# Kernel tuning notes

Hardware: AMD Instinct MI355X
Metric: run time of the kernel (lower is better)

Reference implementation:

```python
import jax, jax.numpy as jnp
import numpy as np

B, N, K = 4, 16384, 8
NF = [8, 32, 64, 128, 256]
E = N * K


def setup_inputs() -> dict:
    key = jax.random.key(0)
    ks = jax.random.split(key, 16)
    x = jax.random.normal(ks[0], (B, N, NF[0]), jnp.float32)
    # knn-style edge list: every node appears as a center K times (no empty segments)
    centers = jnp.tile(jnp.repeat(jnp.arange(N), K)[None, None, :], (B, 1, 1))
    neighbors = jax.random.randint(ks[1], (B, 1, E), 0, N)
    edge_index = jnp.concatenate([centers, neighbors], axis=1)
    specs = [("0a", NF[0], NF[1]), ("0b", NF[0], NF[1]),
             ("1a", NF[1], NF[2]), ("1b", NF[1], NF[2]),
             ("2a", NF[2], NF[3]), ("2b", NF[2], NF[3]),
             ("3a", NF[3], NF[4]), ("3b", NF[3], NF[4]),
             ("cat", NF[1] + NF[2] + NF[3] + NF[4], 1)]
    inp = {"x": x, "edge_index": edge_index}
    for i, (nm, ci, co) in enumerate(specs):
        inp["W" + nm] = jax.random.normal(ks[2 + i], (ci, co), jnp.float32) / np.sqrt(ci)
        inp["g" + nm] = jnp.ones((co,), jnp.float32)   # BN gamma
        inp["b" + nm] = jnp.zeros((co,), jnp.float32)  # BN beta
    inp["bias"] = jnp.zeros((1,), jnp.float32)
    return inp


def _bn(x, g, b):
    # training-mode BatchNorm1d over all rows (GraphBatchNorm1d reduces over batch*num_points)
    m = x.mean(0)
    v = jnp.mean(jnp.square(x - m), 0)  # biased variance, as torch BN uses for normalization
    return g * (x - m) * jax.lax.rsqrt(v + 1e-5) + b


def _mlp(x, W, g, b):
    # Linear(bias=False) -> BN -> LeakyReLU(0.2)
    return jax.nn.leaky_relu(_bn(x @ W, g, b), negative_slope=0.2)


def reference(x, edge_index,
              W0a, g0a, b0a, W0b, g0b, b0b,
              W1a, g1a, b1a, W1b, g1b, b1b,
              W2a, g2a, b2a, W2b, g2b, b2b,
              W3a, g3a, b3a, W3b, g3b, b3b,
              Wcat, gcat, bcat, bias):
    BN = B * N
    xf = x.reshape(BN, NF[0])
    ei = edge_index.transpose(1, 0, 2).reshape(2, -1)  # [2, B*E]
    off = jnp.repeat(jnp.arange(B) * N, E)
    centers = ei[0] + off
    neighbors = ei[1] + off
    segmax = lambda v: jax.ops.segment_max(v, centers, num_segments=BN)
    x0 = _mlp(xf, W0a, g0a, b0a) + segmax(_mlp(xf[neighbors] - xf[centers], W0b, g0b, b0b))
    x1 = _mlp(x0, W1a, g1a, b1a) + segmax(_mlp(x0, W1b, g1b, b1b)[neighbors])
    x2 = _mlp(x1, W2a, g2a, b2a) + segmax(_mlp(x1, W2b, g2b, b2b)[neighbors])
    x3 = _mlp(x2, W3a, g3a, b3a) + segmax(_mlp(x2, W3b, g3b, b3b)[neighbors])
    x_cat = _mlp(jnp.concatenate([x0, x1, x2, x3], axis=-1), Wcat, gcat, bcat)
    return x_cat + bias
```

## Files before the change

kernel.cpp:

```cpp
#include <hip/hip_runtime.h>
#include <math.h>

static constexpr int BB = 4;
static constexpr int NN = 16384;
static constexpr int KK = 8;
static constexpr int EE = 131072;
static constexpr int RR = 65536;
static constexpr int EG = 524288;

static constexpr int SPL = 64;
static constexpr size_t SLOT = (size_t)SPL*512;

static constexpr size_t OFF_X0 = 0;
static constexpr size_t OFF_X1 = OFF_X0 + (size_t)RR*32;
static constexpr size_t OFF_X2 = OFF_X1 + (size_t)RR*64;
static constexpr size_t OFF_X3 = OFF_X2 + (size_t)RR*128;
static constexpr size_t OFF_ZB = OFF_X3 + (size_t)RR*256;
static constexpr size_t OFF_ZC = OFF_ZB + (size_t)RR*128;
static constexpr size_t OFF_S  = OFF_ZC + (size_t)RR;
static constexpr size_t OFF_WP = OFF_S + 9*SLOT;
static constexpr size_t OFF_MX = OFF_WP + 65536;
static constexpr size_t WP1_OFF = 0;
static constexpr size_t WP2_OFF = 4096;
static constexpr size_t WP3_OFF = 4096 + 16384;

__device__ __forceinline__ float lrelu(float x) { return fmaxf(x, 0.2f*x); }

__device__ __forceinline__ unsigned short f2h(float f) {
    _Float16 h = (_Float16)f;
    return *(unsigned short*)&h;
}
__device__ __forceinline__ float h2f(unsigned short u) {
    _Float16 h = *(_Float16*)&u;
    return (float)h;
}

typedef __attribute__((ext_vector_type(8))) _Float16 half8v;
typedef __attribute__((ext_vector_type(8))) unsigned short ushort8v;
typedef __attribute__((ext_vector_type(4))) float float4v;

__global__ __launch_bounds__(256) void k_l0_fused(const float* __restrict__ xf,
                                                  const int* __restrict__ ei,
                                                  const float* __restrict__ Wa,
                                                  const float* __restrict__ Wb,
                                                  const float* __restrict__ gb,
                                                  unsigned short* __restrict__ xa,
                                                  float* __restrict__ mxb,
                                                  float* __restrict__ Sa,
                                                  float* __restrict__ Sb) {
    __shared__ float wa[256], wb[256];
    __shared__ float red[128];
    __shared__ float sgns[32];
    int tid = threadIdx.x;
    wa[tid] = Wa[tid];
    wb[tid] = Wb[tid];
    if (tid < 128) red[tid] = 0.f;
    if (tid < 32) sgns[tid] = (gb[tid] >= 0.f) ? 1.f : -1.f;
    __syncthreads();
    int g = tid & 3, cg = g*8;
    int r = (blockIdx.x*256 + tid) >> 2;
    int b = r >> 14, n = r & (NN-1);
    const int4* nb4 = (const int4*)(ei + (size_t)b*2*EE + EE + n*KK);
    int4 q0v = nb4[0], q1v = nb4[1];
    int nbr[KK] = {q0v.x,q0v.y,q0v.z,q0v.w,q1v.x,q1v.y,q1v.z,q1v.w};
    const float4* pc = (const float4*)(xf + (size_t)r*8);
    float4 c0 = pc[0], c1 = pc[1];
    float xv[8] = {c0.x,c0.y,c0.z,c0.w,c1.x,c1.y,c1.z,c1.w};
    float sgn[8];
#pragma unroll
    for (int j = 0; j < 8; ++j) sgn[j] = sgns[cg+j];

    float4 nA[KK], nB[KK];
#pragma unroll
    for (int k = 0; k < KK; ++k) {
        const float4* pn = (const float4*)(xf + ((size_t)(b<<14) + nbr[k])*8);
        nA[k] = pn[0]; nB[k] = pn[1];
    }

    float opa[8];
#pragma unroll
    for (int j = 0; j < 8; ++j) {
        float s = 0.f;
#pragma unroll
        for (int k = 0; k < 8; ++k) s = fmaf(xv[k], wa[k*32+cg+j], s);
        opa[j] = s;
    }
    {
        ushort8v h;
#pragma unroll
        for (int j = 0; j < 8; ++j) h[j] = f2h(opa[j]);
        *(ushort8v*)&xa[(size_t)r*32 + cg] = h;
    }

    float s8[8], q8[8], mx[8];
#pragma unroll
    for (int j = 0; j < 8; ++j) { s8[j] = 0.f; q8[j] = 0.f; mx[j] = -3.0e38f; }
#pragma unroll
    for (int k = 0; k < KK; ++k) {
        float4 n0 = nA[k], n1 = nB[k];
        float d[8] = {n0.x-xv[0], n0.y-xv[1], n0.z-xv[2], n0.w-xv[3],
                      n1.x-xv[4], n1.y-xv[5], n1.z-xv[6], n1.w-xv[7]};
#pragma unroll
        for (int jj = 0; jj < 8; ++jj) {
            float z = 0.f;
#pragma unroll
            for (int k2 = 0; k2 < 8; ++k2) z = fmaf(d[k2], wb[k2*32+cg+jj], z);
            s8[jj] += z;
            q8[jj] = fmaf(z, z, q8[jj]);
            mx[jj] = fmaxf(mx[jj], sgn[jj]*z);
        }
    }
    {
        float4* mp = (float4*)&mxb[(size_t)r*32 + cg];
        mp[0] = (float4){mx[0],mx[1],mx[2],mx[3]};
        mp[1] = (float4){mx[4],mx[5],mx[6],mx[7]};
    }
    float sa8[8], qa8[8];
#pragma unroll
    for (int j = 0; j < 8; ++j) { sa8[j] = opa[j]; qa8[j] = opa[j]*opa[j]; }
#pragma unroll
    for (int off = 4; off <= 32; off <<= 1) {
#pragma unroll
        for (int j = 0; j < 8; ++j) {
            s8[j]  += __shfl_xor(s8[j],  off, 64);
            q8[j]  += __shfl_xor(q8[j],  off, 64);
            sa8[j] += __shfl_xor(sa8[j], off, 64);
            qa8[j] += __shfl_xor(qa8[j], off, 64);
        }
    }
    if ((tid & 63) < 4) {
#pragma unroll
        for (int j = 0; j < 8; ++j) {
            atomicAdd(&red[cg + j],       sa8[j]);
            atomicAdd(&red[32 + cg + j],  qa8[j]);
            atomicAdd(&red[64 + cg + j],  s8[j]);
            atomicAdd(&red[96 + cg + j],  q8[j]);
        }
    }
    __syncthreads();
    size_t pl = (size_t)(blockIdx.x & (SPL-1))*512;
    if (tid < 64) atomicAdd(&Sa[pl + tid], red[tid]);
    else if (tid < 128) atomicAdd(&Sb[pl + (tid - 64)], red[tid]);
}

__global__ __launch_bounds__(256) void k_edge_apply2(const float* __restrict__ mxb,
                                                     const float* __restrict__ Sa,
                                                     const float* __restrict__ Sb,
                                                     const float* __restrict__ ga,
                                                     const float* __restrict__ ba,
                                                     const float* __restrict__ gb,
                                                     const float* __restrict__ bbp,
                                                     const float* __restrict__ Wc,
                                                     unsigned short* __restrict__ x0,
                                                     float* __restrict__ zc) {
    __shared__ float scbA[32], shb[32], sca[32], sha[32], swc[32];
    int tid = threadIdx.x;
    if (tid < 32) {
        float su = 0.f, qu = 0.f;
        for (int p = 0; p < SPL; ++p) { su += Sa[(size_t)p*512 + tid]; qu += Sa[(size_t)p*512 + 32 + tid]; }
        float m = su*(1.f/RR);
        float v = fmaxf(qu*(1.f/RR) - m*m, 0.f);
        float sc = ga[tid]*rsqrtf(v + 1e-5f);
        sca[tid] = sc; sha[tid] = fmaf(-m, sc, ba[tid]);
        swc[tid] = Wc[tid];
    } else if (tid < 64) {
        int c = tid - 32;
        float su = 0.f, qu = 0.f;
        for (int p = 0; p < SPL; ++p) { su += Sb[(size_t)p*512 + c]; qu += Sb[(size_t)p*512 + 32 + c]; }
        float m = su*(1.f/EG);
        float v = fmaxf(qu*(1.f/EG) - m*m, 0.f);
        float sc = gb[c]*rsqrtf(v + 1e-5f);
        scbA[c] = fabsf(sc);
        shb[c] = fmaf(-m, sc, bbp[c]);
    }
    __syncthreads();
    int r = blockIdx.x*256 + tid;
    ushort8v* xp = (ushort8v*)(x0 + (size_t)r*32);
    const float4* mp = (const float4*)(mxb + (size_t)r*32);
    float sdot = 0.f;
#pragma unroll
    for (int i = 0; i < 4; ++i) {
        ushort8v v = xp[i];
        float4 m0 = mp[i*2], m1 = mp[i*2+1];
        float mx8[8] = {m0.x,m0.y,m0.z,m0.w,m1.x,m1.y,m1.z,m1.w};
        ushort8v o;
#pragma unroll
        for (int j = 0; j < 8; ++j) {
            int c = i*8 + j;
            float y = lrelu(fmaf(mx8[j], scbA[c], shb[c]));
            float val = lrelu(fmaf(h2f(v[j]), sca[c], sha[c])) + y;
            o[j] = f2h(val);
            sdot = fmaf(val, swc[c], sdot);
        }
        xp[i] = o;
    }
    zc[r] = sdot;
}

template<int CI, int CO>
__device__ __forceinline__ void packone(int t, const float* __restrict__ Wa,
                                        const float* __restrict__ Wb,
                                        unsigned short* __restrict__ Wp) {
    constexpr int NT = 2*CO;
    constexpr int KT = CI/32;
    int ng = t % NT, k = t / NT;
    float v = (ng < CO) ? Wa[(size_t)k*CO + ng] : Wb[(size_t)k*CO + (ng - CO)];
    int nt = ng >> 4, n = ng & 15;
    int kt = k >> 5, kq = (k & 31) >> 3, j = k & 7;
    int f = nt*KT + kt;
    int idx = f*512 + ((kq*16 + n)<<3) + j;
    Wp[idx] = f2h(v);
}

__global__ __launch_bounds__(256) void k_prep(const float* __restrict__ W1a, const float* __restrict__ W1b,
                                              const float* __restrict__ W2a, const float* __restrict__ W2b,
                                              const float* __restrict__ W3a, const float* __restrict__ W3b,
                                              unsigned short* __restrict__ wp1,
                                              unsigned short* __restrict__ wp2,
                                              unsigned short* __restrict__ wp3,
                                              float* __restrict__ S) {
    int t = blockIdx.x*256 + threadIdx.x;
    int NT_ = gridDim.x*256;
    for (int u = t; u < (int)(9*SLOT); u += NT_) S[u] = 0.f;
    for (int u = t; u < 32*128;  u += NT_) packone<32,64>(u, W1a, W1b, wp1);
    for (int u = t; u < 64*256;  u += NT_) packone<64,128>(u, W2a, W2b, wp2);
    for (int u = t; u < 128*512; u += NT_) packone<128,256>(u, W3a, W3b, wp3);
}

template<int CI, int CO, int MW>
__global__ __launch_bounds__(256, MW) void k_mfma_dual4(const unsigned short* __restrict__ X,
                                                        const unsigned short* __restrict__ Wp,
                                                        unsigned short* __restrict__ Za,
                                                        unsigned short* __restrict__ Zb,
                                                        float* __restrict__ Sa,
                                                        float* __restrict__ Sb) {
    constexpr int NCH = 4;
    constexpr int KT = CI/32;
    constexpr int WCNT = NCH*KT*512;
    constexpr int ROWT = RR/64;
    constexpr int STR = NCH*16 + 8;
    constexpr int XW  = (CI < 64) ? CI : 64;
    constexpr int PLB = CO/64;
    __shared__ unsigned short scr[4][16*STR];
    int tid = threadIdx.x;
    int lane = tid & 63, wid = tid >> 6;
    int ch = blockIdx.y;
    int wglob = blockIdx.x*4 + wid;
    int NW = gridDim.x*4;
    int n = lane & 15, kq = lane >> 4;
    int rg = lane >> 3, c8l = (lane & 7)*8;
    unsigned short* myscr = scr[wid];
    size_t pl = (size_t)(wglob & (SPL-1)) * 512;
    bool isA = (ch < PLB);
    unsigned short* Zp = (isA ? Za : Zb) + (size_t)(isA ? ch : ch - PLB)*((size_t)RR*64);

    half8v wreg[KT][NCH];
    {
        const unsigned short* Wc = Wp + (size_t)ch*WCNT;
#pragma unroll
        for (int kt = 0; kt < KT; ++kt)
#pragma unroll
            for (int j = 0; j < NCH; ++j)
                wreg[kt][j] = *(const half8v*)&Wc[(j*KT + kt)*512 + lane*8];
    }

    float4v ps[NCH], pq[NCH];
#pragma unroll
    for (int j = 0; j < NCH; ++j) { ps[j] = (float4v){0,0,0,0}; pq[j] = (float4v){0,0,0,0}; }

    auto issue = [&](half8v (&dst)[4], size_t rowb, int kt) {
        int k0 = kt*32 + kq*8;
        int xpl = k0 >> 6;
        int xoff = k0 & (XW-1);
        const unsigned short* Xp = X + (size_t)xpl*((size_t)RR*64);
#pragma unroll
        for (int i = 0; i < 4; ++i)
            dst[i] = *(const half8v*)&Xp[(rowb + i*16 + n)*XW + xoff];
    };

    auto epilogue = [&](float4v (&acc)[4][NCH], size_t rowbase) {
#pragma unroll
        for (int j = 0; j < NCH; ++j)
#pragma unroll
            for (int i = 0; i < 4; ++i) {
                float4v a4 = acc[i][j];
#pragma unroll
                for (int reg = 0; reg < 4; ++reg) {
                    ps[j][reg] += a4[reg];
                    pq[j][reg] = fmaf(a4[reg], a4[reg], pq[j][reg]);
                }
            }
#pragma unroll
        for (int i = 0; i < 4; ++i) {
            __builtin_amdgcn_wave_barrier();
#pragma unroll
            for (int j = 0; j < NCH; ++j) {
                float4v a4 = acc[i][j];
                ushort4 h = { f2h(a4[0]), f2h(a4[1]), f2h(a4[2]), f2h(a4[3]) };
                *(ushort4*)&myscr[n*STR + j*16 + kq*4] = h;
            }
            __builtin_amdgcn_wave_barrier();
#pragma unroll
            for (int i2 = 0; i2 < 2; ++i2) {
                int rit = rg + i2*8;
                ushort8v v = *(const ushort8v*)&myscr[rit*STR + c8l];
                *(ushort8v*)&Zp[(rowbase + i*16 + rit)*64 + c8l] = v;
            }
        }
    };

    if constexpr (KT == 1) {
        for (int t = wglob; t < ROWT; t += NW) {
            size_t rowbase = (size_t)t*64;
            float4v acc[4][NCH];
#pragma unroll
            for (int i = 0; i < 4; ++i)
#pragma unroll
                for (int j = 0; j < NCH; ++j) acc[i][j] = (float4v){0,0,0,0};
            half8v b[4];
            issue(b, rowbase, 0);
#pragma unroll
            for (int j = 0; j < NCH; ++j)
#pragma unroll
                for (int i = 0; i < 4; ++i)
                    acc[i][j] = __builtin_amdgcn_mfma_f32_16x16x32_f16(wreg[0][j], b[i], acc[i][j], 0, 0, 0);
            epilogue(acc, rowbase);
        }
    } else {
        half8v b0[4], b1[4];
        int t = wglob;
        if (t < ROWT) issue(b0, (size_t)t*64, 0);
        for (; t < ROWT; t += NW) {
            size_t rowbase = (size_t)t*64;
            int t2 = t + NW;
            size_t nextrb = (t2 < ROWT) ? (size_t)t2*64 : rowbase;
            float4v acc[4][NCH];
#pragma unroll
            for (int i = 0; i < 4; ++i)
#pragma unroll
                for (int j = 0; j < NCH; ++j) acc[i][j] = (float4v){0,0,0,0};

            auto step = [&](half8v (&bc)[4], half8v (&bn)[4], int kt) {
                if (kt + 1 < KT) issue(bn, rowbase, kt + 1);
                else             issue(bn, nextrb, 0);
#pragma unroll
                for (int j = 0; j < NCH; ++j)
#pragma unroll
                    for (int i = 0; i < 4; ++i)
                        acc[i][j] = __builtin_amdgcn_mfma_f32_16x16x32_f16(wreg[kt][j], bc[i], acc[i][j], 0, 0, 0);
            };
#pragma unroll
            for (int kh = 0; kh < KT/2; ++kh) {
                step(b0, b1, 2*kh);
                step(b1, b0, 2*kh + 1);
            }
            epilogue(acc, rowbase);
        }
    }

    {
        float* Sg = isA ? Sa : Sb;
        int cb0 = isA ? ch*64 : ch*64 - CO;
#pragma unroll
        for (int j = 0; j < NCH; ++j) {
#pragma unroll
            for (int reg = 0; reg < 4; ++reg) {
                float s = ps[j][reg], q = pq[j][reg];
                s += __shfl_xor(s, 1, 64); q += __shfl_xor(q, 1, 64);
                s += __shfl_xor(s, 2, 64); q += __shfl_xor(q, 2, 64);
                s += __shfl_xor(s, 4, 64); q += __shfl_xor(q, 4, 64);
                s += __shfl_xor(s, 8, 64); q += __shfl_xor(q, 8, 64);
                if (n == 0) {
                    int col = cb0 + j*16 + kq*4 + reg;
                    atomicAdd(&Sg[pl + col], s);
                    atomicAdd(&Sg[pl + CO + col], q);
                }
            }
        }
    }
}

template<int CO>
__global__ __launch_bounds__(256) void k_redstats(float* __restrict__ Sa,
                                                  float* __restrict__ Sb) {
    int t = blockIdx.x*256 + threadIdx.x;
    for (int u = t; u < 2*CO; u += gridDim.x*256) {
        float sa = 0.f, sb = 0.f;
        for (int p = 1; p < SPL; ++p) {
            sa += Sa[(size_t)p*512 + u];
            sb += Sb[(size_t)p*512 + u];
        }
        Sa[u] += sa;
        Sb[u] += sb;
    }
}

template<int CO, bool WRITEBACK>
__global__ __launch_bounds__(256) void k_gathermax(unsigned short* __restrict__ xi,
                                                   const unsigned short* __restrict__ zbh,
                                                   const int* __restrict__ ei,
                                                   const float* __restrict__ Sa,
                                                   const float* __restrict__ Sb,
                                                   const float* __restrict__ ga,
                                                   const float* __restrict__ ba,
                                                   const float* __restrict__ gb,
                                                   const float* __restrict__ bbp,
                                                   const float* __restrict__ Wc,
                                                   int wcoff,
                                                   float* __restrict__ zc) {
    constexpr int CQ = CO/8;
    __shared__ float sca[CO], sha[CO], sbA[CO], shb[CO], swc[CO], sgn[CO];
    int tid = threadIdx.x;
    for (int u = tid; u < CO; u += 256) {
        float m = Sa[u]*(1.f/RR);
        float v = fmaxf(Sa[CO+u]*(1.f/RR) - m*m, 0.f);
        float sc = ga[u]*rsqrtf(v + 1e-5f);
        sca[u] = sc; sha[u] = fmaf(-m, sc, ba[u]);
        m = Sb[u]*(1.f/RR);
        v = fmaxf(Sb[CO+u]*(1.f/RR) - m*m, 0.f);
        sc = gb[u]*rsqrtf(v + 1e-5f);
        sbA[u] = fabsf(sc); sgn[u] = (sc >= 0.f) ? 1.f : -1.f;
        shb[u] = fmaf(-m, sc, bbp[u]);
        swc[u] = Wc[wcoff + u];
    }
    __syncthreads();
    int bx = (int)((blockIdx.x & 7)*(gridDim.x >> 3) + (blockIdx.x >> 3));
    int t = bx*256 + tid;
    int r = t / CQ;
    int c8 = (t % CQ)*8;
    int pln = c8 >> 6;
    int off = c8 & 63;
    const unsigned short* zpl = zbh + (size_t)pln*((size_t)RR*64);
    unsigned short* xpl = xi + (size_t)pln*((size_t)RR*64);
    int b = r >> 14, n = r & (NN-1);
    const int4* nb4 = (const int4*)(ei + (size_t)b*2*EE + EE + n*KK);
    int4 q0 = nb4[0], q1 = nb4[1];
    int nbr[KK] = {q0.x,q0.y,q0.z,q0.w,q1.x,q1.y,q1.z,q1.w};
    size_t bb64 = ((size_t)(b<<14))*64 + off;
    ushort8v* xp = (ushort8v*)&xpl[(size_t)r*64 + off];
    ushort8v a = *xp;
    ushort8v u[KK];
#pragma unroll
    for (int k = 0; k < KK; ++k)
        u[k] = *(const ushort8v*)(zpl + bb64 + (size_t)nbr[k]*64);
    float sg[8], sb[8], hb[8];
#pragma unroll
    for (int j = 0; j < 8; ++j) { sg[j] = sgn[c8+j]; sb[j] = sbA[c8+j]; hb[j] = shb[c8+j]; }
    float mx[8];
#pragma unroll
    for (int j = 0; j < 8; ++j) mx[j] = -3e38f;
#pragma unroll
    for (int k = 0; k < KK; ++k)
#pragma unroll
        for (int j = 0; j < 8; ++j)
            mx[j] = fmaxf(mx[j], sg[j]*h2f(u[k][j]));
    float sdot = 0.f;
    if (WRITEBACK) {
        ushort8v o;
#pragma unroll
        for (int j = 0; j < 8; ++j) {
            int c = c8 + j;
            float y = lrelu(fmaf(mx[j], sb[j], hb[j]));
            float val = lrelu(fmaf(h2f(a[j]), sca[c], sha[c])) + y;
            o[j] = f2h(val);
            sdot = fmaf(val, swc[c], sdot);
        }
        *xp = o;
    } else {
#pragma unroll
        for (int j = 0; j < 8; ++j) {
            int c = c8 + j;
            float y = lrelu(fmaf(mx[j], sb[j], hb[j]));
            float val = lrelu(fmaf(h2f(a[j]), sca[c], sha[c])) + y;
            sdot = fmaf(val, swc[c], sdot);
        }
    }
#pragma unroll
    for (int w = CQ/2; w >= 1; w >>= 1) sdot += __shfl_xor(sdot, w, 64);
    int lane = tid & 63;
    if ((lane & (CQ-1)) == 0) atomicAdd(&zc[r], sdot);
}

__global__ __launch_bounds__(256) void k_catstats(const float* __restrict__ zc,
                                                  float* __restrict__ S8) {
    __shared__ float rs2[2];
    int tid = threadIdx.x;
    if (tid < 2) rs2[tid] = 0.f;
    __syncthreads();
    float v = zc[blockIdx.x*256 + tid];
    float s = v, q = v*v;
#pragma unroll
    for (int off = 32; off >= 1; off >>= 1) {
        s += __shfl_xor(s, off, 64);
        q += __shfl_xor(q, off, 64);
    }
    if ((tid & 63) == 0) { atomicAdd(&rs2[0], s); atomicAdd(&rs2[1], q); }
    __syncthreads();
    if (tid == 0) {
        int p = blockIdx.x & 255;
        atomicAdd(&S8[p*2],     rs2[0]);
        atomicAdd(&S8[p*2 + 1], rs2[1]);
    }
}

__global__ __launch_bounds__(256) void k_catfinal(const float* __restrict__ zc,
                                                  const float* __restrict__ S8,
                                                  const float* __restrict__ g,
                                                  const float* __restrict__ bb,
                                                  const float* __restrict__ bias,
                                                  float* __restrict__ out) {
    __shared__ float rs[256], rq[256];
    int tid = threadIdx.x;
    rs[tid] = S8[tid*2];
    rq[tid] = S8[tid*2 + 1];
    __syncthreads();
#pragma unroll
    for (int h = 128; h >= 1; h >>= 1) {
        if (tid < h) { rs[tid] += rs[tid+h]; rq[tid] += rq[tid+h]; }
        __syncthreads();
    }
    int r = blockIdx.x*256 + tid;
    const float invR = 1.f/65536.f;
    float m = rs[0]*invR;
    float v = fmaxf(rq[0]*invR - m*m, 0.f);
    float sc = g[0]*rsqrtf(v + 1e-5f);
    float sh = fmaf(-m, sc, bb[0]);
    float y = lrelu(fmaf(zc[r], sc, sh));
    out[r] = y + bias[0];
}

extern "C" void kernel_launch(void* const* d_in, const int* in_sizes, int n_in,
                              void* d_out, int out_size, void* d_ws, size_t ws_size,
                              hipStream_t stream) {
    const float* x    = (const float*)d_in[0];
    const int*   ei   = (const int*)d_in[1];
    const float* W0a  = (const float*)d_in[2];
    const float* g0a  = (const float*)d_in[3];
    const float* b0a  = (const float*)d_in[4];
    const float* W0b  = (const float*)d_in[5];
    const float* g0b  = (const float*)d_in[6];
    const float* b0b  = (const float*)d_in[7];
    const float* W1a  = (const float*)d_in[8];
    const float* g1a  = (const float*)d_in[9];
    const float* b1a  = (const float*)d_in[10];
    const float* W1b  = (const float*)d_in[11];
    const float* g1b  = (const float*)d_in[12];
    const float* b1b  = (const float*)d_in[13];
    const float* W2a  = (const float*)d_in[14];
    const float* g2a  = (const float*)d_in[15];
    const float* b2a  = (const float*)d_in[16];
    const float* W2b  = (const float*)d_in[17];
    const float* g2b  = (const float*)d_in[18];
    const float* b2b  = (const float*)d_in[19];
    const float* W3a  = (const float*)d_in[20];
    const float* g3a  = (const float*)d_in[21];
    const float* b3a  = (const float*)d_in[22];
    const float* W3b  = (const float*)d_in[23];
    const float* g3b  = (const float*)d_in[24];
    const float* b3b  = (const float*)d_in[25];
    const float* Wcat = (const float*)d_in[26];
    const float* gcat = (const float*)d_in[27];
    const float* bcat = (const float*)d_in[28];
    const float* bias = (const float*)d_in[29];
    float* out = (float*)d_out;

    float* ws = (float*)d_ws;
    unsigned short* x0 = (unsigned short*)(ws + OFF_X0);
    unsigned short* x1 = (unsigned short*)(ws + OFF_X1);
    unsigned short* x2 = (unsigned short*)(ws + OFF_X2);
    unsigned short* x3 = (unsigned short*)(ws + OFF_X3);
    unsigned short* zbh = (unsigned short*)(ws + OFF_ZB);
    float* zc = ws + OFF_ZC;
    float* S  = ws + OFF_S;
    unsigned short* wpbase = (unsigned short*)(ws + OFF_WP);
    unsigned short* wp1 = wpbase + WP1_OFF;
    unsigned short* wp2 = wpbase + WP2_OFF;
    unsigned short* wp3 = wpbase + WP3_OFF;
    float* mxb = ws + OFF_MX;
    auto Sl = [&](int i) { return S + (size_t)i*SLOT; };

    k_prep<<<256, 256, 0, stream>>>(W1a, W1b, W2a, W2b, W3a, W3b, wp1, wp2, wp3, S);

    k_l0_fused<<<RR*4/256, 256, 0, stream>>>(x, ei, W0a, W0b, g0b, x0, mxb, Sl(0), Sl(1));
    k_edge_apply2<<<RR/256, 256, 0, stream>>>(mxb, Sl(0), Sl(1),
                                              g0a, b0a, g0b, b0b, Wcat, x0, zc);

    k_mfma_dual4<32,64,3><<<dim3(256,2), 256, 0, stream>>>(x0, wp1, x1, zbh, Sl(2), Sl(3));
    k_redstats<64><<<4, 256, 0, stream>>>(Sl(2), Sl(3));
    k_gathermax<64,true><<<RR*8/256, 256, 0, stream>>>(x1, zbh, ei, Sl(2), Sl(3),
                                                       g1a, b1a, g1b, b1b, Wcat, 32, zc);

    k_mfma_dual4<64,128,3><<<dim3(128,4), 256, 0, stream>>>(x1, wp2, x2, zbh, Sl(4), Sl(5));
    k_redstats<128><<<4, 256, 0, stream>>>(Sl(4), Sl(5));
    k_gathermax<128,true><<<RR*16/256, 256, 0, stream>>>(x2, zbh, ei, Sl(4), Sl(5),
                                                         g2a, b2a, g2b, b2b, Wcat, 96, zc);

    k_mfma_dual4<128,256,2><<<dim3(64,8), 256, 0, stream>>>(x2, wp3, x3, zbh, Sl(6), Sl(7));
    k_redstats<256><<<4, 256, 0, stream>>>(Sl(6), Sl(7));
    k_gathermax<256,false><<<RR*32/256, 256, 0, stream>>>(x3, zbh, ei, Sl(6), Sl(7),
                                                          g3a, b3a, g3b, b3b, Wcat, 224, zc);

    k_catstats<<<RR/256, 256, 0, stream>>>(zc, Sl(8));
    k_catfinal<<<RR/256, 256, 0, stream>>>(zc, Sl(8), gcat, bcat, bias, out);
}
```

Before: 276.0 us.

## Restructure MFMA load pipelining and use packed fp16 sign-flip max in gather

```diff
diff --git a/kernel.cpp b/kernel.cpp
--- a/kernel.cpp
+++ b/kernel.cpp
@@ -38,6 +38,17 @@
 typedef __attribute__((ext_vector_type(8))) _Float16 half8v;
 typedef __attribute__((ext_vector_type(8))) unsigned short ushort8v;
 typedef __attribute__((ext_vector_type(4))) float float4v;
+
+__device__ __forceinline__ half8v h8max(half8v a, half8v b) {
+#if __has_builtin(__builtin_elementwise_max)
+    return __builtin_elementwise_max(a, b);
+#else
+    half8v r;
+#pragma unroll
+    for (int j = 0; j < 8; ++j) r[j] = (a[j] > b[j]) ? a[j] : b[j];
+    return r;
+#endif
+}
 
 __global__ __launch_bounds__(256) void k_l0_fused(const float* __restrict__ xf,
                                                   const int* __restrict__ ei,
@@ -278,6 +289,14 @@
             dst[i] = *(const half8v*)&Xp[(rowb + i*16 + n)*XW + xoff];
     };
 
+    auto domfma = [&](float4v (&acc)[4][NCH], half8v (&wk)[NCH], half8v (&bc)[4]) {
+#pragma unroll
+        for (int j = 0; j < NCH; ++j)
+#pragma unroll
+            for (int i = 0; i < 4; ++i)
+                acc[i][j] = __builtin_amdgcn_mfma_f32_16x16x32_f16(wk[j], bc[i], acc[i][j], 0, 0, 0);
+    };
+
     auto epilogue = [&](float4v (&acc)[4][NCH], size_t rowbase) {
 #pragma unroll
         for (int j = 0; j < NCH; ++j)
@@ -310,20 +329,53 @@
     };
 
     if constexpr (KT == 1) {
-        for (int t = wglob; t < ROWT; t += NW) {
+        half8v b0[4], b1[4];
+        for (int t = wglob; t < ROWT; t += 2*NW) {
+            int tB = t + NW;
+            size_t rbA = (size_t)t*64;
+            issue(b0, rbA, 0);
+            bool hasB = (tB < ROWT);
+            size_t rbB = hasB ? (size_t)tB*64 : rbA;
+            if (hasB) issue(b1, rbB, 0);
+            {
+                float4v acc[4][NCH];
+#pragma unroll
+                for (int i = 0; i < 4; ++i)
+#pragma unroll
+                    for (int j = 0; j < NCH; ++j) acc[i][j] = (float4v){0,0,0,0};
+                domfma(acc, wreg[0], b0);
+                epilogue(acc, rbA);
+            }
+            if (hasB) {
+                float4v acc[4][NCH];
+#pragma unroll
+                for (int i = 0; i < 4; ++i)
+#pragma unroll
+                    for (int j = 0; j < NCH; ++j) acc[i][j] = (float4v){0,0,0,0};
+                domfma(acc, wreg[0], b1);
+                epilogue(acc, rbB);
+            }
+        }
+    } else if constexpr (KT == 4) {
+        half8v p0[4], p1[4], p2[4], p3[4];
+        int t = wglob;
+        if (t < ROWT) {
+            issue(p0, (size_t)t*64, 0);
+            issue(p1, (size_t)t*64, 1);
+        }
+        for (; t < ROWT; t += NW) {
             size_t rowbase = (size_t)t*64;
+            int t2 = t + NW;
+            size_t nextrb = (t2 < ROWT) ? (size_t)t2*64 : rowbase;
             float4v acc[4][NCH];
 #pragma unroll
             for (int i = 0; i < 4; ++i)
 #pragma unroll
                 for (int j = 0; j < NCH; ++j) acc[i][j] = (float4v){0,0,0,0};
-            half8v b[4];
-            issue(b, rowbase, 0);
-#pragma unroll
-            for (int j = 0; j < NCH; ++j)
-#pragma unroll
-                for (int i = 0; i < 4; ++i)
-                    acc[i][j] = __builtin_amdgcn_mfma_f32_16x16x32_f16(wreg[0][j], b[i], acc[i][j], 0, 0, 0);
+            issue(p2, rowbase, 2);  domfma(acc, wreg[0], p0);
+            issue(p3, rowbase, 3);  domfma(acc, wreg[1], p1);
+            issue(p0, nextrb, 0);   domfma(acc, wreg[2], p2);
+            issue(p1, nextrb, 1);   domfma(acc, wreg[3], p3);
             epilogue(acc, rowbase);
         }
     } else {
@@ -339,21 +391,8 @@
             for (int i = 0; i < 4; ++i)
 #pragma unroll
                 for (int j = 0; j < NCH; ++j) acc[i][j] = (float4v){0,0,0,0};
-
-            auto step = [&](half8v (&bc)[4], half8v (&bn)[4], int kt) {
-                if (kt + 1 < KT) issue(bn, rowbase, kt + 1);
-                else             issue(bn, nextrb, 0);
-#pragma unroll
-                for (int j = 0; j < NCH; ++j)
-#pragma unroll
-                    for (int i = 0; i < 4; ++i)
-                        acc[i][j] = __builtin_amdgcn_mfma_f32_16x16x32_f16(wreg[kt][j], bc[i], acc[i][j], 0, 0, 0);
-            };
-#pragma unroll
-            for (int kh = 0; kh < KT/2; ++kh) {
-                step(b0, b1, 2*kh);
-                step(b1, b0, 2*kh + 1);
-            }
+            issue(b1, rowbase, 1);  domfma(acc, wreg[0], b0);
+            issue(b0, nextrb, 0);   domfma(acc, wreg[1], b1);
             epilogue(acc, rowbase);
         }
     }
@@ -409,7 +448,8 @@
                                                    int wcoff,
                                                    float* __restrict__ zc) {
     constexpr int CQ = CO/8;
-    __shared__ float sca[CO], sha[CO], sbA[CO], shb[CO], swc[CO], sgn[CO];
+    __shared__ float sca[CO], sha[CO], sbA[CO], shb[CO], swc[CO];
+    __shared__ __attribute__((aligned(16))) unsigned short smk[CO];
     int tid = threadIdx.x;
     for (int u = tid; u < CO; u += 256) {
         float m = Sa[u]*(1.f/RR);
@@ -419,7 +459,8 @@
         m = Sb[u]*(1.f/RR);
         v = fmaxf(Sb[CO+u]*(1.f/RR) - m*m, 0.f);
         sc = gb[u]*rsqrtf(v + 1e-5f);
-        sbA[u] = fabsf(sc); sgn[u] = (sc >= 0.f) ? 1.f : -1.f;
+        sbA[u] = fabsf(sc);
+        smk[u] = (sc >= 0.f) ? (unsigned short)0 : (unsigned short)0x8000;
         shb[u] = fmaf(-m, sc, bbp[u]);
         swc[u] = Wc[wcoff + u];
     }
@@ -443,24 +484,24 @@
 #pragma unroll
     for (int k = 0; k < KK; ++k)
         u[k] = *(const ushort8v*)(zpl + bb64 + (size_t)nbr[k]*64);
-    float sg[8], sb[8], hb[8];
-#pragma unroll
-    for (int j = 0; j < 8; ++j) { sg[j] = sgn[c8+j]; sb[j] = sbA[c8+j]; hb[j] = shb[c8+j]; }
-    float mx[8];
-#pragma unroll
-    for (int j = 0; j < 8; ++j) mx[j] = -3e38f;
-#pragma unroll
-    for (int k = 0; k < KK; ++k)
-#pragma unroll
-        for (int j = 0; j < 8; ++j)
-            mx[j] = fmaxf(mx[j], sg[j]*h2f(u[k][j]));
+    ushort8v msk8 = *(const ushort8v*)&smk[c8];
+    ushort8v ninfu = {0xFC00,0xFC00,0xFC00,0xFC00,0xFC00,0xFC00,0xFC00,0xFC00};
+    half8v mh = __builtin_bit_cast(half8v, ninfu);
+#pragma unroll
+    for (int k = 0; k < KK; ++k) {
+        ushort8v uk = u[k] ^ msk8;
+        mh = h8max(mh, __builtin_bit_cast(half8v, uk));
+    }
+    float sb[8], hb[8];
+#pragma unroll
+    for (int j = 0; j < 8; ++j) { sb[j] = sbA[c8+j]; hb[j] = shb[c8+j]; }
     float sdot = 0.f;
     if (WRITEBACK) {
         ushort8v o;
 #pragma unroll
         for (int j = 0; j < 8; ++j) {
             int c = c8 + j;
-            float y = lrelu(fmaf(mx[j], sb[j], hb[j]));
+            float y = lrelu(fmaf((float)mh[j], sb[j], hb[j]));
             float val = lrelu(fmaf(h2f(a[j]), sca[c], sha[c])) + y;
             o[j] = f2h(val);
             sdot = fmaf(val, swc[c], sdot);
@@ -470,7 +511,7 @@
 #pragma unroll
         for (int j = 0; j < 8; ++j) {
             int c = c8 + j;
-            float y = lrelu(fmaf(mx[j], sb[j], hb[j]));
+            float y = lrelu(fmaf((float)mh[j], sb[j], hb[j]));
             float val = lrelu(fmaf(h2f(a[j]), sca[c], sha[c])) + y;
             sdot = fmaf(val, swc[c], sdot);
         }
@@ -585,7 +626,7 @@
     k_edge_apply2<<<RR/256, 256, 0, stream>>>(mxb, Sl(0), Sl(1),
                                               g0a, b0a, g0b, b0b, Wcat, x0, zc);
 
-    k_mfma_dual4<32,64,3><<<dim3(256,2), 256, 0, stream>>>(x0, wp1, x1, zbh, Sl(2), Sl(3));
+    k_mfma_dual4<32,64,3><<<dim3(128,2), 256, 0, stream>>>(x0, wp1, x1, zbh, Sl(2), Sl(3));
     k_redstats<64><<<4, 256, 0, stream>>>(Sl(2), Sl(3));
     k_gathermax<64,true><<<RR*8/256, 256, 0, stream>>>(x1, zbh, ei, Sl(2), Sl(3),
                                                        g1a, b1a, g1b, b1b, Wcat, 32, zc);
```

Result: no change. 276.8 us (+0.3%).
